# Kernel tuning notes

Measured on AMD Instinct MI355X. Metric: run time of the kernel, lower is better.

The kernel has to match this reference:

```python
import jax, jax.numpy as jnp
import numpy as np

N = 50000
E = 800000
F_IN = 128
HID = 8
HEADS1 = 8
OUT2 = 32
NUM_GRAPHS = 64
NEG_SLOPE = 0.2


def setup_inputs() -> dict:
    key = jax.random.key(0)
    ks = jax.random.split(key, 16)
    x = jax.random.normal(ks[0], (N, F_IN), dtype=jnp.float32)
    edge_index = jax.random.randint(ks[1], (2, E), 0, N, dtype=jnp.int64)
    batch = jnp.sort(jax.random.randint(ks[2], (N,), 0, NUM_GRAPHS, dtype=jnp.int64))
    s = 0.1
    W1 = jax.random.normal(ks[3], (F_IN, HEADS1 * HID), dtype=jnp.float32) * s
    a1_src = jax.random.normal(ks[4], (HEADS1, HID), dtype=jnp.float32) * s
    a1_dst = jax.random.normal(ks[5], (HEADS1, HID), dtype=jnp.float32) * s
    b1 = jnp.zeros((HEADS1 * HID,), dtype=jnp.float32)
    W2 = jax.random.normal(ks[6], (HEADS1 * HID, OUT2), dtype=jnp.float32) * s
    a2_src = jax.random.normal(ks[7], (1, OUT2), dtype=jnp.float32) * s
    a2_dst = jax.random.normal(ks[8], (1, OUT2), dtype=jnp.float32) * s
    b2 = jnp.zeros((OUT2,), dtype=jnp.float32)
    Wlin = jax.random.normal(ks[9], (OUT2, 2), dtype=jnp.float32) * s
    blin = jnp.zeros((2,), dtype=jnp.float32)
    return {"x": x, "edge_index": edge_index, "batch": batch,
            "W1": W1, "a1_src": a1_src, "a1_dst": a1_dst, "b1": b1,
            "W2": W2, "a2_src": a2_src, "a2_dst": a2_dst, "b2": b2,
            "Wlin": Wlin, "blin": blin}


def gat_conv(x, src, dst, W, a_src, a_dst, b, heads, out_ch, concat):
    # x: [N, F]; project per head: [N, H, C]
    h = (x @ W).reshape(N, heads, out_ch)
    # per-node attention halves: [N, H]
    al_s = jnp.einsum('nhc,hc->nh', h, a_src)
    al_d = jnp.einsum('nhc,hc->nh', h, a_dst)
    # per-edge logits (PyG: src contributes a_src term, dst the a_dst term)
    e = jax.nn.leaky_relu(al_s[src] + al_d[dst], NEG_SLOPE)  # [E', H]
    # segment softmax over incoming edges of each dst node
    m = jax.ops.segment_max(e, dst, num_segments=N)
    ex = jnp.exp(e - m[dst])
    denom = jax.ops.segment_sum(ex, dst, num_segments=N)
    alpha = ex / (denom[dst] + 1e-16)  # [E', H]
    # weighted scatter-add of source features
    out = jax.ops.segment_sum(h[src] * alpha[..., None], dst, num_segments=N)  # [N, H, C]
    out = out.reshape(N, heads * out_ch) if concat else out.mean(axis=1)
    return out + b


def reference(x, edge_index, batch, W1, a1_src, a1_dst, b1, W2, a2_src, a2_dst, b2, Wlin, blin):
    # add self-loops (PyG GATConv default add_self_loops=True)
    loops = jnp.arange(N, dtype=edge_index.dtype)
    src = jnp.concatenate([edge_index[0], loops])
    dst = jnp.concatenate([edge_index[1], loops])
    # dropouts are identity in eval mode
    h = gat_conv(x, src, dst, W1, a1_src, a1_dst, b1, HEADS1, HID, True)
    h = jax.nn.elu(h)
    h = gat_conv(h, src, dst, W2, a2_src, a2_dst, b2, 1, OUT2, False)
    # global mean pool over graphs
    sums = jax.ops.segment_sum(h, batch, num_segments=NUM_GRAPHS)
    cnt = jax.ops.segment_sum(jnp.ones((N, 1), h.dtype), batch, num_segments=NUM_GRAPHS)
    pooled = sums / jnp.maximum(cnt, 1.0)
    return pooled @ Wlin + blin
```

## Files before the change

### kernel.cpp

```cpp
#include <hip/hip_runtime.h>
#include <hip/hip_fp16.h>

#define NN 50000
#define EE 800000
#define ETOT (EE + NN)
#define NEG 0.2f
#define NG 64

__device__ __forceinline__ float lrelu(float x) { return x > 0.f ? x : NEG * x; }
__device__ __forceinline__ unsigned fenc(float f) {
    unsigned u = __float_as_uint(f);
    return (u & 0x80000000u) ? ~u : (u | 0x80000000u);
}
__device__ __forceinline__ float fdec(unsigned u) {
    return (u & 0x80000000u) ? __uint_as_float(u & 0x7fffffffu)
                             : __uint_as_float(~u);
}

__global__ __launch_bounds__(256) void gemm1(const float* __restrict__ x,
                                             const float* __restrict__ W1,
                                             const float* __restrict__ a1s,
                                             const float* __restrict__ a1d,
                                             __half* __restrict__ h1h,
                                             float* __restrict__ al1s,
                                             float* __restrict__ al1d) {
    __shared__ float sx[64][132];
    __shared__ float sW[64][64];
    const int t = threadIdx.x;
    const int row0 = blockIdx.x * 64;
    for (int i = t * 4; i < 64 * 128; i += 256 * 4) {
        int r = i >> 7, k = i & 127;
        int gr = row0 + r;
        float4 v = make_float4(0.f, 0.f, 0.f, 0.f);
        if (gr < NN) v = *(const float4*)&x[(size_t)gr * 128 + k];
        *(float4*)&sx[r][k] = v;
    }
    float acc[4][4] = {{0.f, 0.f, 0.f, 0.f}};
    const int c4 = (t & 15) * 4;
    const int r4 = (t >> 4) * 4;
    for (int k0 = 0; k0 < 128; k0 += 64) {
        __syncthreads();
        for (int i = t * 4; i < 64 * 64; i += 256 * 4) {
            int kk = i >> 6, c = i & 63;
            *(float4*)&sW[kk][c] = *(const float4*)&W1[(size_t)(k0 + kk) * 64 + c];
        }
        __syncthreads();
#pragma unroll 4
        for (int kk = 0; kk < 64; kk += 4) {
            float4 wv0 = *(float4*)&sW[kk + 0][c4];
            float4 wv1 = *(float4*)&sW[kk + 1][c4];
            float4 wv2 = *(float4*)&sW[kk + 2][c4];
            float4 wv3 = *(float4*)&sW[kk + 3][c4];
#pragma unroll
            for (int r = 0; r < 4; ++r) {
                float4 xv = *(const float4*)&sx[r4 + r][k0 + kk];
                acc[r][0] += xv.x * wv0.x; acc[r][1] += xv.x * wv0.y; acc[r][2] += xv.x * wv0.z; acc[r][3] += xv.x * wv0.w;
                acc[r][0] += xv.y * wv1.x; acc[r][1] += xv.y * wv1.y; acc[r][2] += xv.y * wv1.z; acc[r][3] += xv.y * wv1.w;
                acc[r][0] += xv.z * wv2.x; acc[r][1] += xv.z * wv2.y; acc[r][2] += xv.z * wv2.z; acc[r][3] += xv.z * wv2.w;
                acc[r][0] += xv.w * wv3.x; acc[r][1] += xv.w * wv3.y; acc[r][2] += xv.w * wv3.z; acc[r][3] += xv.w * wv3.w;
            }
        }
    }
    const float4 asv = *(const float4*)&a1s[c4];
    const float4 adv = *(const float4*)&a1d[c4];
#pragma unroll
    for (int r = 0; r < 4; ++r) {
        int row = row0 + r4 + r;
        float ps = acc[r][0] * asv.x + acc[r][1] * asv.y + acc[r][2] * asv.z + acc[r][3] * asv.w;
        float pd = acc[r][0] * adv.x + acc[r][1] * adv.y + acc[r][2] * adv.z + acc[r][3] * adv.w;
        ps += __shfl_xor(ps, 1);
        pd += __shfl_xor(pd, 1);
        if (row < NN) {
            __half2 h01 = __floats2half2_rn(acc[r][0], acc[r][1]);
            __half2 h23 = __floats2half2_rn(acc[r][2], acc[r][3]);
            float2 pk;
            *(__half2*)&pk.x = h01;
            *(__half2*)&pk.y = h23;
            *(float2*)&h1h[(size_t)row * 64 + c4] = pk;
            if ((t & 1) == 0) {
                int h = (t & 15) >> 1;
                al1s[row * 8 + h] = ps;
                al1d[row * 8 + h] = pd;
            }
        }
    }
}

__global__ __launch_bounds__(256) void maxal1(const float* __restrict__ al1s,
                                              unsigned* __restrict__ gmax1) {
    const int t = blockIdx.x * 256 + threadIdx.x;
    const int h = t & 7;
    float m = -1e30f;
    for (int i = t; i < NN * 8; i += 98 * 256) m = fmaxf(m, al1s[i]);
    m = fmaxf(m, __shfl_xor(m, 8));
    m = fmaxf(m, __shfl_xor(m, 16));
    m = fmaxf(m, __shfl_xor(m, 32));
    if ((threadIdx.x & 63) < 8) atomicMax(&gmax1[h], fenc(m));
}

__global__ __launch_bounds__(256) void hist(const int* __restrict__ ei,
                                            int* __restrict__ deg,
                                            int* __restrict__ epos) {
    int e = blockIdx.x * 256 + threadIdx.x;
    if (e >= ETOT) return;
    int d = (e < EE) ? ei[EE + e] : e - EE;
    epos[e] = atomicAdd(&deg[d], 1);
}

__global__ __launch_bounds__(256) void scan1(const int* __restrict__ deg,
                                             int* __restrict__ rowptr,
                                             int* __restrict__ bsum) {
    __shared__ int s[256];
    int t = threadIdx.x;
    int i = blockIdx.x * 256 + t;
    int v = (i < NN) ? deg[i] : 0;
    s[t] = v;
    __syncthreads();
    for (int off = 1; off < 256; off <<= 1) {
        int u = (t >= off) ? s[t - off] : 0;
        __syncthreads();
        s[t] += u;
        __syncthreads();
    }
    if (i < NN) rowptr[i] = s[t] - v;
    if (t == 255) bsum[blockIdx.x] = s[255];
}

__global__ __launch_bounds__(256) void scan23(int* __restrict__ rowptr,
                                              const int* __restrict__ bsum) {
    __shared__ int soff;
    const int B = blockIdx.x;
    if (threadIdx.x < 64) {
        int sacc = 0;
        for (int idx = threadIdx.x; idx < B; idx += 64) sacc += bsum[idx];
#pragma unroll
        for (int off = 1; off < 64; off <<= 1) sacc += __shfl_xor(sacc, off);
        if (threadIdx.x == 0) soff = sacc;
    }
    __syncthreads();
    int i = B * 256 + threadIdx.x;
    if (i < NN) rowptr[i] += soff;
    if (i == NN) rowptr[NN] = ETOT;
}

__global__ __launch_bounds__(256) void fillcsr(const int* __restrict__ ei,
                                               const int* __restrict__ rowptr,
                                               const int* __restrict__ epos,
                                               int* __restrict__ csr) {
    int e = blockIdx.x * 256 + threadIdx.x;
    if (e >= ETOT) return;
    int s, d;
    if (e < EE) { s = ei[e]; d = ei[EE + e]; } else { s = d = e - EE; }
    csr[rowptr[d] + epos[e]] = s;
}

__global__ __launch_bounds__(256) void maxal2(const float* __restrict__ al2s,
                                              unsigned* __restrict__ gmax2) {
    const int t = blockIdx.x * 256 + threadIdx.x;
    float m = -1e30f;
    for (int i = t; i < NN; i += 98 * 256) m = fmaxf(m, al2s[i]);
#pragma unroll
    for (int off = 32; off; off >>= 1) m = fmaxf(m, __shfl_xor(m, off));
    if ((threadIdx.x & 63) == 0) atomicMax(gmax2, fenc(m));
}

__global__ __launch_bounds__(256) void agg1f(const int* __restrict__ rowptr,
                                             const int* __restrict__ csr,
                                             const float* __restrict__ al1s,
                                             const float* __restrict__ al1d,
                                             const unsigned* __restrict__ gmax1,
                                             const __half* __restrict__ h1h,
                                             const float* __restrict__ b1,
                                             const float* __restrict__ W2,
                                             const float* __restrict__ a2s,
                                             const float* __restrict__ a2d,
                                             __half* __restrict__ h2h,
                                             float* __restrict__ al2s,
                                             float* __restrict__ al2d) {
    const int lane = threadIdx.x & 63;
    const int wid  = blockIdx.x * 4 + (threadIdx.x >> 6);
    const int NW   = gridDim.x * 4;
    const int u  = lane & 15;
    const int g  = lane >> 4;
    const int hh = u >> 1;
    const int c = lane & 31, halfk = lane >> 5;
    float w2r[32];
#pragma unroll
    for (int j = 0; j < 32; ++j) w2r[j] = W2[(size_t)(halfk * 32 + j) * 32 + c];
    const float a2sc = a2s[c], a2dc = a2d[c];
    const float4 b14 = *(const float4*)&b1[u * 4];
    const float M0 = fdec(gmax1[hh]);

    for (int d = wid; d < NN; d += NW) {
        const int beg = rowptr[d], end = rowptr[d + 1];
        const float ald = al1d[d * 8 + hh];
        const float M = lrelu(M0 + ald);
        float den = 0.f;
        float4 a4 = make_float4(0.f, 0.f, 0.f, 0.f);
        for (int base = beg; base < end; base += 64) {
            int cnt = min(64, end - base);
            int myedge = (base + lane < end) ? csr[base + lane] : 0;
            for (int tt = 0; 4 * tt < cnt; ++tt) {
                int j = 4 * tt + g;
                bool valid = j < cnt;
                int jj = valid ? j : cnt - 1;
                int s = __shfl(myedge, jj);
                float al = al1s[s * 8 + hh];
                float2 raw = *(const float2*)&h1h[(size_t)s * 64 + u * 4];
                float2 f01 = __half22float2(*(__half2*)&raw.x);
                float2 f23 = __half22float2(*(__half2*)&raw.y);
                float a = valid ? __expf(lrelu(al + ald) - M) : 0.f;
                den += a;
                a4.x += a * f01.x; a4.y += a * f01.y;
                a4.z += a * f23.x; a4.w += a * f23.y;
            }
        }
        den += __shfl_xor(den, 16); den += __shfl_xor(den, 32);
        a4.x += __shfl_xor(a4.x, 16); a4.x += __shfl_xor(a4.x, 32);
        a4.y += __shfl_xor(a4.y, 16); a4.y += __shfl_xor(a4.y, 32);
        a4.z += __shfl_xor(a4.z, 16); a4.z += __shfl_xor(a4.z, 32);
        a4.w += __shfl_xor(a4.w, 16); a4.w += __shfl_xor(a4.w, 32);
        const float inv = 1.f / (den + 1e-16f);
        float4 v4;
        v4.x = a4.x * inv + b14.x; v4.y = a4.y * inv + b14.y;
        v4.z = a4.z * inv + b14.z; v4.w = a4.w * inv + b14.w;
        v4.x = v4.x > 0.f ? v4.x : (__expf(v4.x) - 1.f);
        v4.y = v4.y > 0.f ? v4.y : (__expf(v4.y) - 1.f);
        v4.z = v4.z > 0.f ? v4.z : (__expf(v4.z) - 1.f);
        v4.w = v4.w > 0.f ? v4.w : (__expf(v4.w) - 1.f);
        float t0 = __shfl(v4.x, lane >> 2);
        float t1 = __shfl(v4.y, lane >> 2);
        float t2 = __shfl(v4.z, lane >> 2);
        float t3 = __shfl(v4.w, lane >> 2);
        int q = lane & 3;
        float v = (q == 0) ? t0 : (q == 1) ? t1 : (q == 2) ? t2 : t3;
        float acc2 = 0.f;
        const int kb = lane & 32;
#pragma unroll
        for (int j = 0; j < 32; ++j) acc2 += __shfl(v, kb + j) * w2r[j];
        acc2 += __shfl_xor(acc2, 32);
        float ps = acc2 * a2sc, pd = acc2 * a2dc;
#pragma unroll
        for (int off = 1; off < 32; off <<= 1) {
            ps += __shfl_xor(ps, off);
            pd += __shfl_xor(pd, off);
        }
        if (lane == 0) { al2s[d] = ps; al2d[d] = pd; }
        if (halfk == 0) h2h[(size_t)d * 32 + c] = __float2half(acc2);
    }
}

__global__ __launch_bounds__(256) void agg2(const int* __restrict__ rowptr,
                                            const int* __restrict__ csr,
                                            const float* __restrict__ al2s,
                                            const float* __restrict__ al2d,
                                            const unsigned* __restrict__ gmax2,
                                            const __half* __restrict__ h2h,
                                            float* __restrict__ out2) {
    const int lane = threadIdx.x & 63;
    const int d = blockIdx.x * 4 + (threadIdx.x >> 6);
    if (d >= NN) return;
    const int u = lane & 7;
    const int g = lane >> 3;
    const int beg = rowptr[d], end = rowptr[d + 1];
    const float ald = al2d[d];
    const float M = lrelu(fdec(gmax2[0]) + ald);
    float den = 0.f;
    float4 a4 = make_float4(0.f, 0.f, 0.f, 0.f);
    for (int base = beg; base < end; base += 64) {
        int cnt = min(64, end - base);
        int myedge = (base + lane < end) ? csr[base + lane] : 0;
        for (int tt = 0; 8 * tt < cnt; ++tt) {
            int j = 8 * tt + g;
            bool valid = j < cnt;
            int jj = valid ? j : cnt - 1;
            int s = __shfl(myedge, jj);
            float al = al2s[s];
            float2 raw = *(const float2*)&h2h[(size_t)s * 32 + u * 4];
            float2 f01 = __half22float2(*(__half2*)&raw.x);
            float2 f23 = __half22float2(*(__half2*)&raw.y);
            float a = valid ? __expf(lrelu(al + ald) - M) : 0.f;
            den += a;
            a4.x += a * f01.x; a4.y += a * f01.y;
            a4.z += a * f23.x; a4.w += a * f23.y;
        }
    }
    den += __shfl_xor(den, 8); den += __shfl_xor(den, 16); den += __shfl_xor(den, 32);
    a4.x += __shfl_xor(a4.x, 8); a4.x += __shfl_xor(a4.x, 16); a4.x += __shfl_xor(a4.x, 32);
    a4.y += __shfl_xor(a4.y, 8); a4.y += __shfl_xor(a4.y, 16); a4.y += __shfl_xor(a4.y, 32);
    a4.z += __shfl_xor(a4.z, 8); a4.z += __shfl_xor(a4.z, 16); a4.z += __shfl_xor(a4.z, 32);
    a4.w += __shfl_xor(a4.w, 8); a4.w += __shfl_xor(a4.w, 16); a4.w += __shfl_xor(a4.w, 32);
    if (g == 0) {
        const float inv = 1.f / (den + 1e-16f);
        *(float4*)&out2[(size_t)d * 32 + u * 4] =
            make_float4(a4.x * inv, a4.y * inv, a4.z * inv, a4.w * inv);
    }
}

__global__ __launch_bounds__(256) void pool(const float* __restrict__ out2,
                                            const float* __restrict__ b2,
                                            const int* __restrict__ batch,
                                            float* __restrict__ psum,
                                            float* __restrict__ pcnt) {
    __shared__ float sacc[8][32];
    __shared__ float scnt[8];
    const int t = threadIdx.x;
    const int c = t & 31, sl = t >> 5;
    const int n0 = blockIdx.x * 256;
    const int g0 = batch[n0 < NN ? n0 : NN - 1];
    float acc = 0.f, cnt = 0.f;
    for (int k = 0; k < 32; ++k) {
        int n = n0 + sl + 8 * k;
        if (n < NN) {
            float v = out2[(size_t)n * 32 + c] + b2[c];
            int g = batch[n];
            if (g == g0) {
                acc += v;
                if (c == 0) cnt += 1.f;
            } else {
                atomicAdd(&psum[g * 32 + c], v);
                if (c == 0) atomicAdd(&pcnt[g], 1.f);
            }
        }
    }
    sacc[sl][c] = acc;
    if (c == 0) scnt[sl] = cnt;
    __syncthreads();
    if (t < 32) {
        float s = 0.f;
        for (int j = 0; j < 8; ++j) s += sacc[j][t];
        atomicAdd(&psum[g0 * 32 + t], s);
        if (t == 0) {
            float sc = 0.f;
            for (int j = 0; j < 8; ++j) sc += scnt[j];
            atomicAdd(&pcnt[g0], sc);
        }
    }
}

__global__ __launch_bounds__(128) void final_lin(const float* __restrict__ psum,
                                                 const float* __restrict__ pcnt,
                                                 const float* __restrict__ Wlin,
                                                 const float* __restrict__ blin,
                                                 float* __restrict__ out) {
    int t = threadIdx.x;
    if (t >= NG * 2) return;
    int g = t >> 1, j = t & 1;
    float cnt = fmaxf(pcnt[g], 1.0f);
    float acc = blin[j];
    for (int c = 0; c < 32; ++c) acc += (psum[g * 32 + c] / cnt) * Wlin[c * 2 + j];
    out[g * 2 + j] = acc;
}

static inline size_t alignup(size_t x) { return (x + 255) & ~(size_t)255; }

extern "C" void kernel_launch(void* const* d_in, const int* in_sizes, int n_in,
                              void* d_out, int out_size, void* d_ws, size_t ws_size,
                              hipStream_t stream) {
    const float* x    = (const float*)d_in[0];
    const int*   ei   = (const int*)d_in[1];
    const int*   batch= (const int*)d_in[2];
    const float* W1   = (const float*)d_in[3];
    const float* a1s  = (const float*)d_in[4];
    const float* a1d  = (const float*)d_in[5];
    const float* b1   = (const float*)d_in[6];
    const float* W2   = (const float*)d_in[7];
    const float* a2s  = (const float*)d_in[8];
    const float* a2d  = (const float*)d_in[9];
    const float* b2   = (const float*)d_in[10];
    const float* Wlin = (const float*)d_in[11];
    const float* blin = (const float*)d_in[12];
    float* out = (float*)d_out;
    char* ws = (char*)d_ws;
    (void)in_sizes; (void)n_in; (void)out_size; (void)ws_size;

    size_t o = 0;
    size_t DEG  = o; o += alignup((size_t)NN * 4);
    size_t PSUM = o; o += alignup((size_t)NG * 32 * 4);
    size_t PCNT = o; o += alignup((size_t)NG * 4);
    size_t GMX1 = o; o += alignup(8 * 4);
    size_t GMX2 = o; o += alignup(4);
    size_t zero_bytes = o;
    size_t ROWP = o; o += alignup((size_t)(NN + 1) * 4);
    size_t BSUM = o; o += alignup((size_t)256 * 4);
    size_t EPOS = o; o += alignup((size_t)ETOT * 4);
    size_t CSR  = o; o += alignup((size_t)ETOT * 4 + 256);
    size_t H1H  = o; o += alignup((size_t)NN * 64 * 2);
    size_t AL1S = o; o += alignup((size_t)NN * 8 * 4);
    size_t AL1D = o; o += alignup((size_t)NN * 8 * 4);
    size_t H2H  = o; o += alignup((size_t)NN * 32 * 2);
    size_t AL2S = o; o += alignup((size_t)NN * 4);
    size_t AL2D = o; o += alignup((size_t)NN * 4);
    size_t OUT2 = o; o += alignup((size_t)NN * 32 * 4);

    int*      deg    = (int*)(ws + DEG);
    float*    psum   = (float*)(ws + PSUM);
    float*    pcnt   = (float*)(ws + PCNT);
    unsigned* gmax1  = (unsigned*)(ws + GMX1);
    unsigned* gmax2  = (unsigned*)(ws + GMX2);
    int*      rowptr = (int*)(ws + ROWP);
    int*      bsum   = (int*)(ws + BSUM);
    int*      epos   = (int*)(ws + EPOS);
    int*      csr    = (int*)(ws + CSR);
    __half*   h1h    = (__half*)(ws + H1H);
    float*    al1s_  = (float*)(ws + AL1S);
    float*    al1d_  = (float*)(ws + AL1D);
    __half*   h2h    = (__half*)(ws + H2H);
    float*    al2s   = (float*)(ws + AL2S);
    float*    al2d   = (float*)(ws + AL2D);
    float*    out2   = (float*)(ws + OUT2);

    hipMemsetAsync(ws, 0, zero_bytes, stream);

    gemm1<<<(NN + 63) / 64, 256, 0, stream>>>(x, W1, a1s, a1d, h1h, al1s_, al1d_);

    const int gE = (ETOT + 255) / 256;
    const int nbScan = (NN + 255) / 256;
    hist<<<gE, 256, 0, stream>>>(ei, deg, epos);
    scan1<<<nbScan, 256, 0, stream>>>(deg, rowptr, bsum);
    scan23<<<(NN + 256) / 256, 256, 0, stream>>>(rowptr, bsum);
    fillcsr<<<gE, 256, 0, stream>>>(ei, rowptr, epos, csr);

    maxal1<<<98, 256, 0, stream>>>(al1s_, gmax1);

    agg1f<<<2048, 256, 0, stream>>>(rowptr, csr, al1s_, al1d_, gmax1, h1h,
                                    b1, W2, a2s, a2d, h2h, al2s, al2d);

    maxal2<<<98, 256, 0, stream>>>(al2s, gmax2);

    const int gN = (NN + 3) / 4;
    agg2<<<gN, 256, 0, stream>>>(rowptr, csr, al2s, al2d, gmax2, h2h, out2);

    pool<<<(NN + 255) / 256, 256, 0, stream>>>(out2, b2, batch, psum, pcnt);

    final_lin<<<1, 128, 0, stream>>>(psum, pcnt, Wlin, blin, out);
}
```

Before: 237.2 us.

## Fuse histogram into GEMM launch, max into CSR fill, and narrow CSR to 16-bit

Runs the degree histogram in extra blocks of the first GEMM launch, and the layer-1 attention max in extra blocks of the CSR fill kernel, removing two launches and letting independent work share the GPU. It also stores edge positions and CSR source indices as unsigned short to halve their memory traffic. Node ids go up to 49999, which fits in 16 bits, but per-node degree positions also rely on staying below 65536. The narrower indices make the code specific to this graph size.

```diff
diff --git a/kernel.cpp b/kernel.cpp
--- a/kernel.cpp
+++ b/kernel.cpp
@@ -6,6 +6,8 @@
 #define ETOT (EE + NN)
 #define NEG 0.2f
 #define NG 64
+#define HISTB 256
+#define MAXB 98
 
 __device__ __forceinline__ float lrelu(float x) { return x > 0.f ? x : NEG * x; }
 __device__ __forceinline__ unsigned fenc(float f) {
@@ -17,17 +19,27 @@
                              : __uint_as_float(~u);
 }
 
-__global__ __launch_bounds__(256) void gemm1(const float* __restrict__ x,
-                                             const float* __restrict__ W1,
-                                             const float* __restrict__ a1s,
-                                             const float* __restrict__ a1d,
-                                             __half* __restrict__ h1h,
-                                             float* __restrict__ al1s,
-                                             float* __restrict__ al1d) {
+__global__ __launch_bounds__(256) void gemm1h(const float* __restrict__ x,
+                                              const float* __restrict__ W1,
+                                              const float* __restrict__ a1s,
+                                              const float* __restrict__ a1d,
+                                              __half* __restrict__ h1h,
+                                              float* __restrict__ al1s,
+                                              float* __restrict__ al1d,
+                                              const int* __restrict__ ei,
+                                              int* __restrict__ deg,
+                                              unsigned short* __restrict__ epos) {
     __shared__ float sx[64][132];
     __shared__ float sW[64][64];
     const int t = threadIdx.x;
-    const int row0 = blockIdx.x * 64;
+    if (blockIdx.x < HISTB) {
+        for (long long e = (long long)blockIdx.x * 256 + t; e < ETOT; e += (long long)HISTB * 256) {
+            int d = (e < EE) ? ei[EE + e] : (int)(e - EE);
+            epos[e] = (unsigned short)atomicAdd(&deg[d], 1);
+        }
+        return;
+    }
+    const int row0 = (blockIdx.x - HISTB) * 64;
     for (int i = t * 4; i < 64 * 128; i += 256 * 4) {
         int r = i >> 7, k = i & 127;
         int gr = row0 + r;
@@ -86,27 +98,6 @@
     }
 }
 
-__global__ __launch_bounds__(256) void maxal1(const float* __restrict__ al1s,
-                                              unsigned* __restrict__ gmax1) {
-    const int t = blockIdx.x * 256 + threadIdx.x;
-    const int h = t & 7;
-    float m = -1e30f;
-    for (int i = t; i < NN * 8; i += 98 * 256) m = fmaxf(m, al1s[i]);
-    m = fmaxf(m, __shfl_xor(m, 8));
-    m = fmaxf(m, __shfl_xor(m, 16));
-    m = fmaxf(m, __shfl_xor(m, 32));
-    if ((threadIdx.x & 63) < 8) atomicMax(&gmax1[h], fenc(m));
-}
-
-__global__ __launch_bounds__(256) void hist(const int* __restrict__ ei,
-                                            int* __restrict__ deg,
-                                            int* __restrict__ epos) {
-    int e = blockIdx.x * 256 + threadIdx.x;
-    if (e >= ETOT) return;
-    int d = (e < EE) ? ei[EE + e] : e - EE;
-    epos[e] = atomicAdd(&deg[d], 1);
-}
-
 __global__ __launch_bounds__(256) void scan1(const int* __restrict__ deg,
                                              int* __restrict__ rowptr,
                                              int* __restrict__ bsum) {
@@ -143,15 +134,28 @@
     if (i == NN) rowptr[NN] = ETOT;
 }
 
-__global__ __launch_bounds__(256) void fillcsr(const int* __restrict__ ei,
+__global__ __launch_bounds__(256) void fillmax(const int* __restrict__ ei,
                                                const int* __restrict__ rowptr,
-                                               const int* __restrict__ epos,
-                                               int* __restrict__ csr) {
-    int e = blockIdx.x * 256 + threadIdx.x;
+                                               const unsigned short* __restrict__ epos,
+                                               unsigned short* __restrict__ csr,
+                                               const float* __restrict__ al1s,
+                                               unsigned* __restrict__ gmax1) {
+    if (blockIdx.x < MAXB) {
+        const int t = blockIdx.x * 256 + threadIdx.x;
+        const int h = t & 7;
+        float m = -1e30f;
+        for (int i = t; i < NN * 8; i += MAXB * 256) m = fmaxf(m, al1s[i]);
+        m = fmaxf(m, __shfl_xor(m, 8));
+        m = fmaxf(m, __shfl_xor(m, 16));
+        m = fmaxf(m, __shfl_xor(m, 32));
+        if ((threadIdx.x & 63) < 8) atomicMax(&gmax1[h], fenc(m));
+        return;
+    }
+    int e = (blockIdx.x - MAXB) * 256 + threadIdx.x;
     if (e >= ETOT) return;
     int s, d;
     if (e < EE) { s = ei[e]; d = ei[EE + e]; } else { s = d = e - EE; }
-    csr[rowptr[d] + epos[e]] = s;
+    csr[rowptr[d] + epos[e]] = (unsigned short)s;
 }
 
 __global__ __launch_bounds__(256) void maxal2(const float* __restrict__ al2s,
@@ -165,7 +169,7 @@
 }
 
 __global__ __launch_bounds__(256) void agg1f(const int* __restrict__ rowptr,
-                                             const int* __restrict__ csr,
+                                             const unsigned short* __restrict__ csr,
                                              const float* __restrict__ al1s,
                                              const float* __restrict__ al1d,
                                              const unsigned* __restrict__ gmax1,
@@ -199,7 +203,7 @@
         float4 a4 = make_float4(0.f, 0.f, 0.f, 0.f);
         for (int base = beg; base < end; base += 64) {
             int cnt = min(64, end - base);
-            int myedge = (base + lane < end) ? csr[base + lane] : 0;
+            int myedge = (base + lane < end) ? (int)csr[base + lane] : 0;
             for (int tt = 0; 4 * tt < cnt; ++tt) {
                 int j = 4 * tt + g;
                 bool valid = j < cnt;
@@ -251,7 +255,7 @@
 }
 
 __global__ __launch_bounds__(256) void agg2(const int* __restrict__ rowptr,
-                                            const int* __restrict__ csr,
+                                            const unsigned short* __restrict__ csr,
                                             const float* __restrict__ al2s,
                                             const float* __restrict__ al2d,
                                             const unsigned* __restrict__ gmax2,
@@ -269,7 +273,7 @@
     float4 a4 = make_float4(0.f, 0.f, 0.f, 0.f);
     for (int base = beg; base < end; base += 64) {
         int cnt = min(64, end - base);
-        int myedge = (base + lane < end) ? csr[base + lane] : 0;
+        int myedge = (base + lane < end) ? (int)csr[base + lane] : 0;
         for (int tt = 0; 8 * tt < cnt; ++tt) {
             int j = 8 * tt + g;
             bool valid = j < cnt;
@@ -383,8 +387,8 @@
     size_t zero_bytes = o;
     size_t ROWP = o; o += alignup((size_t)(NN + 1) * 4);
     size_t BSUM = o; o += alignup((size_t)256 * 4);
-    size_t EPOS = o; o += alignup((size_t)ETOT * 4);
-    size_t CSR  = o; o += alignup((size_t)ETOT * 4 + 256);
+    size_t EPOS = o; o += alignup((size_t)ETOT * 2);
+    size_t CSR  = o; o += alignup((size_t)ETOT * 2 + 256);
     size_t H1H  = o; o += alignup((size_t)NN * 64 * 2);
     size_t AL1S = o; o += alignup((size_t)NN * 8 * 4);
     size_t AL1D = o; o += alignup((size_t)NN * 8 * 4);
@@ -393,35 +397,35 @@
     size_t AL2D = o; o += alignup((size_t)NN * 4);
     size_t OUT2 = o; o += alignup((size_t)NN * 32 * 4);
 
-    int*      deg    = (int*)(ws + DEG);
-    float*    psum   = (float*)(ws + PSUM);
-    float*    pcnt   = (float*)(ws + PCNT);
-    unsigned* gmax1  = (unsigned*)(ws + GMX1);
-    unsigned* gmax2  = (unsigned*)(ws + GMX2);
-    int*      rowptr = (int*)(ws + ROWP);
-    int*      bsum   = (int*)(ws + BSUM);
-    int*      epos   = (int*)(ws + EPOS);
-    int*      csr    = (int*)(ws + CSR);
-    __half*   h1h    = (__half*)(ws + H1H);
-    float*    al1s_  = (float*)(ws + AL1S);
-    float*    al1d_  = (float*)(ws + AL1D);
-    __half*   h2h    = (__half*)(ws + H2H);
-    float*    al2s   = (float*)(ws + AL2S);
-    float*    al2d   = (float*)(ws + AL2D);
-    float*    out2   = (float*)(ws + OUT2);
+    int*            deg    = (int*)(ws + DEG);
+    float*          psum   = (float*)(ws + PSUM);
+    float*          pcnt   = (float*)(ws + PCNT);
+    unsigned*       gmax1  = (unsigned*)(ws + GMX1);
+    unsigned*       gmax2  = (unsigned*)(ws + GMX2);
+    int*            rowptr = (int*)(ws + ROWP);
+    int*            bsum   = (int*)(ws + BSUM);
+    unsigned short* epos   = (unsigned short*)(ws + EPOS);
+    unsigned short* csr    = (unsigned short*)(ws + CSR);
+    __half*         h1h    = (__half*)(ws + H1H);
+    float*          al1s_  = (float*)(ws + AL1S);
+    float*          al1d_  = (float*)(ws + AL1D);
+    __half*         h2h    = (__half*)(ws + H2H);
+    float*          al2s   = (float*)(ws + AL2S);
+    float*          al2d   = (float*)(ws + AL2D);
+    float*          out2   = (float*)(ws + OUT2);
 
     hipMemsetAsync(ws, 0, zero_bytes, stream);
 
-    gemm1<<<(NN + 63) / 64, 256, 0, stream>>>(x, W1, a1s, a1d, h1h, al1s_, al1d_);
-
-    const int gE = (ETOT + 255) / 256;
+    const int gemmB = (NN + 63) / 64;
+    gemm1h<<<HISTB + gemmB, 256, 0, stream>>>(x, W1, a1s, a1d, h1h, al1s_, al1d_,
+                                              ei, deg, epos);
+
     const int nbScan = (NN + 255) / 256;
-    hist<<<gE, 256, 0, stream>>>(ei, deg, epos);
     scan1<<<nbScan, 256, 0, stream>>>(deg, rowptr, bsum);
     scan23<<<(NN + 256) / 256, 256, 0, stream>>>(rowptr, bsum);
-    fillcsr<<<gE, 256, 0, stream>>>(ei, rowptr, epos, csr);
-
-    maxal1<<<98, 256, 0, stream>>>(al1s_, gmax1);
+
+    const int gE = (ETOT + 255) / 256;
+    fillmax<<<MAXB + gE, 256, 0, stream>>>(ei, rowptr, epos, csr, al1s_, gmax1);
 
     agg1f<<<2048, 256, 0, stream>>>(rowptr, csr, al1s_, al1d_, gmax1, h1h,
                                     b1, W2, a2s, a2d, h2h, al2s, al2d);
```

Measured after the change: 223.6 us. 1.06x faster.
